# Kernel tuning notes

Measured on AMD Instinct MI355X. Metric: run time of the kernel, lower is better.

The kernel has to match this reference:

```python
import jax, jax.numpy as jnp
import numpy as np
from jax import lax
from jax.scipy.special import logsumexp

B, T, K = 256, 1024, 64


def setup_inputs() -> dict:
    key = jax.random.key(0)
    k1, k2, k3 = jax.random.split(key, 3)
    y_true = jax.random.randint(k1, (B, T), 0, K)  # 0 == pad tag
    emissions = jax.random.normal(k2, (B, T, K), dtype=jnp.float32)
    transition = jax.random.normal(k3, (K, K), dtype=jnp.float32) * 0.1
    return {"y_true": y_true, "emissions": emissions, "transition": transition}


def _log_partition(emissions, mask, transition):
    # alpha_0 = emissions[:, 0, :] (TF code does not mask step 0)
    alpha0 = emissions[:, 0, :]  # [B, K]

    def step(alpha, xs):
        emit_t, m_t = xs  # [B, K], [B]
        # score[b, i, j] = alpha[b, i] + transition[i, j] + emit_t[b, j]
        score = alpha[:, :, None] + transition[None, :, :] + emit_t[:, None, :]
        new_a = logsumexp(score, axis=1)  # [B, K]
        new_a = jnp.where(m_t[:, None] > 0, new_a, alpha)
        return new_a, None

    xs = (jnp.swapaxes(emissions[:, 1:, :], 0, 1),  # [T-1, B, K]
          jnp.swapaxes(mask[:, 1:], 0, 1))           # [T-1, B]
    alpha, _ = lax.scan(step, alpha0, xs)
    return logsumexp(alpha, axis=1)  # [B]


def reference(y_true, emissions, transition):
    mask = (y_true != 0).astype(emissions.dtype)  # [B, T]
    yt = y_true.astype(jnp.int32)

    # emission scores of the gold path on masked emissions
    em_masked = emissions * mask[:, :, None]
    e_scores = jnp.take_along_axis(em_masked, yt[:, :, None], axis=2)[..., 0].sum(axis=1)  # [B]

    # transition scores of the gold path
    prev, nxt = yt[:, :-1], yt[:, 1:]
    t_scores = (transition[prev, nxt] * mask[:, 1:]).sum(axis=1)  # [B]

    log_z = _log_partition(emissions, mask, transition)  # [B]
    ll = e_scores + t_scores - log_z
    return -jnp.mean(ll)
```

## Files before the change

kernel.cpp:

```cpp
#include <hip/hip_runtime.h>

#define LOG2E 1.44269504088896340736f
#define LN2   0.69314718055994530942f

typedef short bf8 __attribute__((ext_vector_type(8)));
typedef float f4  __attribute__((ext_vector_type(4)));
typedef float v2f __attribute__((ext_vector_type(2)));

static __device__ __forceinline__ unsigned short f2bf_rne(float f) {
    unsigned u = __float_as_uint(f);
    u += 0x7FFFu + ((u >> 16) & 1u);
    return (unsigned short)(u >> 16);
}
static __device__ __forceinline__ unsigned pack_bf_trunc(float lo, float hi) {
    return __builtin_amdgcn_perm(__float_as_uint(hi), __float_as_uint(lo), 0x07060302u);
}

__global__ __attribute__((amdgpu_flat_work_group_size(64, 64), amdgpu_waves_per_eu(1, 4)))
void crf_scan(const int* __restrict__ yg, const float* __restrict__ em,
              const float* __restrict__ tr, unsigned short* __restrict__ Pg)
{
    constexpr int T = 1024, STR = 72;
    const int c = blockIdx.x, b = blockIdx.y;
    const int lane = threadIdx.x, nl = lane & 15, q = lane >> 4;

    __shared__ __align__(16) unsigned short p_sh[64 * STR];
    __shared__ __align__(16) float d_sh[64];

    #pragma unroll
    for (int r = 0; r < 9; ++r) {
        uint4 z; z.x = z.y = z.z = z.w = 0u;
        *(uint4*)&p_sh[lane * STR + r * 8] = z;
    }
    p_sh[lane * STR + lane] = 0x3F80;

    bf8 afr[4][2];
    #pragma unroll
    for (int mt = 0; mt < 4; ++mt)
        #pragma unroll
        for (int kt = 0; kt < 2; ++kt) {
            bf8 v;
            #pragma unroll
            for (int j = 0; j < 8; ++j) {
                const int k = 32 * kt + 8 * q + j, m = 16 * mt + nl;
                v[j] = (short)f2bf_rne(exp2f(tr[k * 64 + m] * LOG2E));
            }
            afr[mt][kt] = v;
        }

    const int t0 = 1 + 64 * c;
    const int nsteps = (c == 15) ? 63 : 64;
    const float* emb = em + (size_t)b * T * 64;

    int tl = t0 + lane; if (tl > T - 1) tl = T - 1;
    const int yvl = yg[b * T + tl];
    const unsigned long long msk = __ballot(lane < nsteps && yvl != 0);

    const f4 zf4 = {0.f, 0.f, 0.f, 0.f};

    float ldc = emb[t0 * 64 + lane];
    for (int s = 0; s < nsteps; ++s) {
        int tn = t0 + s + 1; if (tn > T - 1) tn = T - 1;
        const float ldn = emb[tn * 64 + lane];
        if ((msk >> s) & 1ull) {
            d_sh[lane] = exp2f(ldc * LOG2E - 7.0f);
            bf8 bfr[2][4];
            #pragma unroll
            for (int kt = 0; kt < 2; ++kt)
                #pragma unroll
                for (int nt = 0; nt < 4; ++nt)
                    bfr[kt][nt] = *(const bf8*)&p_sh[(16 * nt + nl) * STR + 32 * kt + 8 * q];
            v2f d01[4], d23[4];
            #pragma unroll
            for (int mt = 0; mt < 4; ++mt) {
                const f4 dv = *(const f4*)&d_sh[16 * mt + 4 * q];
                d01[mt] = (v2f){dv[0], dv[1]};
                d23[mt] = (v2f){dv[2], dv[3]};
            }
            #pragma unroll
            for (int mt = 0; mt < 4; ++mt)
                #pragma unroll
                for (int nt = 0; nt < 4; ++nt) {
                    f4 acc = __builtin_amdgcn_mfma_f32_16x16x32_bf16(
                                 afr[mt][0], bfr[0][nt], zf4, 0, 0, 0);
                    acc = __builtin_amdgcn_mfma_f32_16x16x32_bf16(
                                 afr[mt][1], bfr[1][nt], acc, 0, 0, 0);
                    const v2f lo = (v2f){acc[0], acc[1]} * d01[mt];
                    const v2f hi = (v2f){acc[2], acc[3]} * d23[mt];
                    uint2 w;
                    w.x = pack_bf_trunc(lo.x, lo.y);
                    w.y = pack_bf_trunc(hi.x, hi.y);
                    *(uint2*)&p_sh[(16 * nt + nl) * STR + 16 * mt + 4 * q] = w;
                }
        }
        ldc = ldn;
    }

    unsigned short* pg = Pg + ((size_t)(b * 16 + c) << 12);
    #pragma unroll
    for (int r = 0; r < 8; ++r)
        *(uint4*)(pg + lane * 64 + r * 8) = *(const uint4*)&p_sh[lane * STR + r * 8];
}

__global__ __attribute__((amdgpu_flat_work_group_size(64, 64), amdgpu_waves_per_eu(1, 1)))
void crf_combine(const int* __restrict__ yg, const float* __restrict__ em,
                 const float* __restrict__ tr, const unsigned short* __restrict__ Pg,
                 float* __restrict__ out)
{
    constexpr int T = 1024;
    const int b = blockIdx.x, j = threadIdx.x;
    __shared__ __align__(16) float v_sh[64];

    const float e0 = em[(size_t)b * T * 64 + j];
    float M0 = e0;
    #pragma unroll
    for (int o = 32; o > 0; o >>= 1) M0 = fmaxf(M0, __shfl_xor(M0, o, 64));
    float v = exp2f((e0 - M0) * LOG2E);
    float L = M0;

    const int* yb = yg + b * T;
    int cnt = 0; float ep = 0.f, tp = 0.f;
    for (int t = 1 + j; t < T; t += 64) {
        const int yt = yb[t];
        if (yt != 0) {
            ++cnt;
            tp += tr[yb[t - 1] * 64 + yt];
            ep += em[((size_t)b * T + t) * 64 + yt];
        }
    }
    if (j == 0) {
        const int y0 = yb[0];
        if (y0 != 0) ep += em[(size_t)b * T * 64 + y0];
    }

    const unsigned short* pgb = Pg + ((size_t)(b * 16) << 12) + j * 64;
    uint4 r0, r1, r2, r3, r4, r5, r6, r7;
    {
        const uint4* p = (const uint4*)pgb;
        r0 = p[0]; r1 = p[1]; r2 = p[2]; r3 = p[3];
        r4 = p[4]; r5 = p[5]; r6 = p[6]; r7 = p[7];
    }
    for (int c = 0; c < 16; ++c) {
        uint4 n0, n1, n2, n3, n4, n5, n6, n7;
        if (c < 15) {
            const uint4* p = (const uint4*)(pgb + ((size_t)(c + 1) << 12));
            n0 = p[0]; n1 = p[1]; n2 = p[2]; n3 = p[3];
            n4 = p[4]; n5 = p[5]; n6 = p[6]; n7 = p[7];
        }
        v_sh[j] = v;
        float s0 = 0.f, s1 = 0.f, s2 = 0.f, s3 = 0.f;
        const uint4 qs[8] = {r0, r1, r2, r3, r4, r5, r6, r7};
        #pragma unroll
        for (int r = 0; r < 8; ++r) {
            const uint4 qq = qs[r];
            const float* vp = &v_sh[r * 8];
            s0 = fmaf(__uint_as_float(qq.x << 16),         vp[0], s0);
            s1 = fmaf(__uint_as_float(qq.x & 0xFFFF0000u), vp[1], s1);
            s2 = fmaf(__uint_as_float(qq.y << 16),         vp[2], s2);
            s3 = fmaf(__uint_as_float(qq.y & 0xFFFF0000u), vp[3], s3);
            s0 = fmaf(__uint_as_float(qq.z << 16),         vp[4], s0);
            s1 = fmaf(__uint_as_float(qq.z & 0xFFFF0000u), vp[5], s1);
            s2 = fmaf(__uint_as_float(qq.w << 16),         vp[6], s2);
            s3 = fmaf(__uint_as_float(qq.w & 0xFFFF0000u), vp[7], s3);
        }
        float s = (s0 + s1) + (s2 + s3);
        const unsigned sb = (unsigned)__builtin_amdgcn_readlane((int)__float_as_uint(s), 0);
        const int ef = (int)((sb >> 23) & 0xFF);
        if (ef > 0 && ef < 255 && ef != 127) {
            const int E = ef - 127;
            s *= __uint_as_float((unsigned)(127 - E) << 23);
            L += (float)E * LN2;
        }
        v = s;
        if (c < 15) {
            r0 = n0; r1 = n1; r2 = n2; r3 = n3;
            r4 = n4; r5 = n5; r6 = n6; r7 = n7;
        }
    }

    float vs = v, eps = ep, tps = tp; int cs = cnt;
    #pragma unroll
    for (int o = 32; o > 0; o >>= 1) {
        vs  += __shfl_xor(vs, o, 64);
        eps += __shfl_xor(eps, o, 64);
        tps += __shfl_xor(tps, o, 64);
        cs  += __shfl_xor(cs, o, 64);
    }
    if (j == 0) {
        const float logz = L + 7.0f * LN2 * (float)cs + __log2f(vs) * LN2;
        const float ll = eps + tps - logz;
        atomicAdd(out, ll * (-1.0f / 256.0f));
    }
}

extern "C" void kernel_launch(void* const* d_in, const int* in_sizes, int n_in,
                              void* d_out, int out_size, void* d_ws, size_t ws_size,
                              hipStream_t stream) {
    const int*   y  = (const int*)d_in[0];
    const float* em = (const float*)d_in[1];
    const float* tr = (const float*)d_in[2];
    float* out = (float*)d_out;
    unsigned short* Pg = (unsigned short*)d_ws;

    hipMemsetAsync(out, 0, sizeof(float), stream);
    crf_scan<<<dim3(16, 256), dim3(64), 0, stream>>>(y, em, tr, Pg);
    crf_combine<<<dim3(256), dim3(64), 0, stream>>>(y, em, tr, Pg, out);
}
```

Baseline: 252.1 us.

## Split CRF scan into 32 chunks and XOR-swizzle shared P matrix

The time axis is cut into 32 chunks of 32 steps when the workspace is large enough, instead of 16 chunks of 64. This doubles the number of workgroups and halves the serial chain per block, and waves_per_eu is raised to allow more occupancy. The padded-stride LDS layout is replaced by an XOR swizzle to avoid bank conflicts without padding. In exchange, the combine kernel now does twice as many serial 64x64 matrix-vector steps and reads twice as much workspace, and the extra bf16 chunk products may add rounding error.

```diff
diff --git a/kernel.cpp b/kernel.cpp
--- a/kernel.cpp
+++ b/kernel.cpp
@@ -16,23 +16,25 @@
     return __builtin_amdgcn_perm(__float_as_uint(hi), __float_as_uint(lo), 0x07060302u);
 }
 
-__global__ __attribute__((amdgpu_flat_work_group_size(64, 64), amdgpu_waves_per_eu(1, 4)))
+template <int CH>
+__global__ __attribute__((amdgpu_flat_work_group_size(64, 64), amdgpu_waves_per_eu(1, 8)))
 void crf_scan(const int* __restrict__ yg, const float* __restrict__ em,
               const float* __restrict__ tr, unsigned short* __restrict__ Pg)
 {
-    constexpr int T = 1024, STR = 72;
+    constexpr int T = 1024, STEPS = T / CH;
     const int c = blockIdx.x, b = blockIdx.y;
     const int lane = threadIdx.x, nl = lane & 15, q = lane >> 4;
-
-    __shared__ __align__(16) unsigned short p_sh[64 * STR];
+    const int swz = lane & 7;
+
+    __shared__ __align__(16) unsigned short p_sh[64 * 64];
     __shared__ __align__(16) float d_sh[64];
 
     #pragma unroll
-    for (int r = 0; r < 9; ++r) {
+    for (int r = 0; r < 8; ++r) {
         uint4 z; z.x = z.y = z.z = z.w = 0u;
-        *(uint4*)&p_sh[lane * STR + r * 8] = z;
-    }
-    p_sh[lane * STR + lane] = 0x3F80;
+        *(uint4*)&p_sh[lane * 64 + r * 8] = z;
+    }
+    p_sh[lane * 64 + (((lane >> 3) ^ swz) << 3) + (lane & 7)] = 0x3F80;
 
     bf8 afr[4][2];
     #pragma unroll
@@ -48,13 +50,12 @@
             afr[mt][kt] = v;
         }
 
-    const int t0 = 1 + 64 * c;
-    const int nsteps = (c == 15) ? 63 : 64;
+    const int t0 = 1 + STEPS * c;
+    const int nsteps = (c == CH - 1) ? STEPS - 1 : STEPS;
     const float* emb = em + (size_t)b * T * 64;
 
     int tl = t0 + lane; if (tl > T - 1) tl = T - 1;
-    const int yvl = yg[b * T + tl];
-    const unsigned long long msk = __ballot(lane < nsteps && yvl != 0);
+    const unsigned long long msk = __ballot(lane < nsteps && yg[b * T + tl] != 0);
 
     const f4 zf4 = {0.f, 0.f, 0.f, 0.f};
 
@@ -69,7 +70,8 @@
             for (int kt = 0; kt < 2; ++kt)
                 #pragma unroll
                 for (int nt = 0; nt < 4; ++nt)
-                    bfr[kt][nt] = *(const bf8*)&p_sh[(16 * nt + nl) * STR + 32 * kt + 8 * q];
+                    bfr[kt][nt] = *(const bf8*)
+                        &p_sh[(16 * nt + nl) * 64 + (((4 * kt + q) ^ swz) << 3)];
             v2f d01[4], d23[4];
             #pragma unroll
             for (int mt = 0; mt < 4; ++mt) {
@@ -90,18 +92,22 @@
                     uint2 w;
                     w.x = pack_bf_trunc(lo.x, lo.y);
                     w.y = pack_bf_trunc(hi.x, hi.y);
-                    *(uint2*)&p_sh[(16 * nt + nl) * STR + 16 * mt + 4 * q] = w;
+                    *(uint2*)&p_sh[(16 * nt + nl) * 64 +
+                                   (((2 * mt + (q >> 1)) ^ swz) << 3) +
+                                   ((q & 1) << 2)] = w;
                 }
         }
         ldc = ldn;
     }
 
-    unsigned short* pg = Pg + ((size_t)(b * 16 + c) << 12);
+    unsigned short* pg = Pg + ((size_t)(b * CH + c) << 12);
     #pragma unroll
     for (int r = 0; r < 8; ++r)
-        *(uint4*)(pg + lane * 64 + r * 8) = *(const uint4*)&p_sh[lane * STR + r * 8];
-}
-
+        *(uint4*)(pg + lane * 64 + r * 8) =
+            *(const uint4*)&p_sh[lane * 64 + ((r ^ swz) << 3)];
+}
+
+template <int CH>
 __global__ __attribute__((amdgpu_flat_work_group_size(64, 64), amdgpu_waves_per_eu(1, 1)))
 void crf_combine(const int* __restrict__ yg, const float* __restrict__ em,
                  const float* __restrict__ tr, const unsigned short* __restrict__ Pg,
@@ -133,26 +139,25 @@
         if (y0 != 0) ep += em[(size_t)b * T * 64 + y0];
     }
 
-    const unsigned short* pgb = Pg + ((size_t)(b * 16) << 12) + j * 64;
-    uint4 r0, r1, r2, r3, r4, r5, r6, r7;
+    const unsigned short* pgb = Pg + ((size_t)b * CH << 12) + j * 64;
+    uint4 cur[8];
     {
         const uint4* p = (const uint4*)pgb;
-        r0 = p[0]; r1 = p[1]; r2 = p[2]; r3 = p[3];
-        r4 = p[4]; r5 = p[5]; r6 = p[6]; r7 = p[7];
-    }
-    for (int c = 0; c < 16; ++c) {
-        uint4 n0, n1, n2, n3, n4, n5, n6, n7;
-        if (c < 15) {
+        #pragma unroll
+        for (int r = 0; r < 8; ++r) cur[r] = p[r];
+    }
+    for (int c = 0; c < CH; ++c) {
+        uint4 nxt[8];
+        if (c < CH - 1) {
             const uint4* p = (const uint4*)(pgb + ((size_t)(c + 1) << 12));
-            n0 = p[0]; n1 = p[1]; n2 = p[2]; n3 = p[3];
-            n4 = p[4]; n5 = p[5]; n6 = p[6]; n7 = p[7];
+            #pragma unroll
+            for (int r = 0; r < 8; ++r) nxt[r] = p[r];
         }
         v_sh[j] = v;
         float s0 = 0.f, s1 = 0.f, s2 = 0.f, s3 = 0.f;
-        const uint4 qs[8] = {r0, r1, r2, r3, r4, r5, r6, r7};
         #pragma unroll
         for (int r = 0; r < 8; ++r) {
-            const uint4 qq = qs[r];
+            const uint4 qq = cur[r];
             const float* vp = &v_sh[r * 8];
             s0 = fmaf(__uint_as_float(qq.x << 16),         vp[0], s0);
             s1 = fmaf(__uint_as_float(qq.x & 0xFFFF0000u), vp[1], s1);
@@ -172,9 +177,9 @@
             L += (float)E * LN2;
         }
         v = s;
-        if (c < 15) {
-            r0 = n0; r1 = n1; r2 = n2; r3 = n3;
-            r4 = n4; r5 = n5; r6 = n6; r7 = n7;
+        if (c < CH - 1) {
+            #pragma unroll
+            for (int r = 0; r < 8; ++r) cur[r] = nxt[r];
         }
     }
 
@@ -203,6 +208,12 @@
     unsigned short* Pg = (unsigned short*)d_ws;
 
     hipMemsetAsync(out, 0, sizeof(float), stream);
-    crf_scan<<<dim3(16, 256), dim3(64), 0, stream>>>(y, em, tr, Pg);
-    crf_combine<<<dim3(256), dim3(64), 0, stream>>>(y, em, tr, Pg, out);
-}
+    const size_t need32 = (size_t)256 * 32 * 4096 * 2;
+    if (ws_size >= need32) {
+        crf_scan<32><<<dim3(32, 256), dim3(64), 0, stream>>>(y, em, tr, Pg);
+        crf_combine<32><<<dim3(256), dim3(64), 0, stream>>>(y, em, tr, Pg, out);
+    } else {
+        crf_scan<16><<<dim3(16, 256), dim3(64), 0, stream>>>(y, em, tr, Pg);
+        crf_combine<16><<<dim3(256), dim3(64), 0, stream>>>(y, em, tr, Pg, out);
+    }
+}
```

New measurement: 256.5 us. Within noise of the previous version (+1.8%).
